# Kernel optimization log

Hardware: AMD Instinct MI355X
Metric: run time of the kernel (lower is better)

The kernel has to match this reference:

```python
import jax, jax.numpy as jnp
import numpy as np

LOOKBACK = 8
EPS = 1e-6
HID = 32
MV_DIM = 11  # 1 scalar + 4 vector + 6 bivector
# default bivector planes (i, j)
BIV_I = jnp.array([0, 0, 0, 1, 1, 2])
BIV_J = jnp.array([1, 2, 3, 2, 3, 3])


def phi(x):
    # LeakyReLU(x, 0.01) + 1.0
    return jnp.where(x >= 0, x, 0.01 * x) + 1.0


def setup_inputs() -> dict:
    key = jax.random.key(0)
    ks = jax.random.split(key, 10)
    B, L = 8, 16384
    return {
        "x": jax.random.normal(ks[0], (B, L, 4), dtype=jnp.float32),
        "scalar_bias": jax.random.normal(ks[1], (1,), dtype=jnp.float32) * 0.1,
        "vector_scale": 1.0 + jax.random.normal(ks[2], (4,), dtype=jnp.float32) * 0.1,
        "vector_bias": jax.random.normal(ks[3], (4,), dtype=jnp.float32) * 0.1,
        "bivector_weight": 1.0 + jax.random.normal(ks[4], (6,), dtype=jnp.float32) * 0.1,
        "W_Q": jax.random.normal(ks[5], (MV_DIM, HID), dtype=jnp.float32) * 0.3,
        "W_K": jax.random.normal(ks[6], (MV_DIM, HID), dtype=jnp.float32) * 0.3,
        "W_V": jax.random.normal(ks[7], (MV_DIM, HID), dtype=jnp.float32) * 0.3,
        "w_head": jax.random.normal(ks[8], (HID,), dtype=jnp.float32) * 0.18,
        "b_head": jax.random.normal(ks[9], (), dtype=jnp.float32) * 0.1,
    }


def ga_embed(x, scalar_bias, vector_scale, vector_bias, bivector_weight):
    B, L, _ = x.shape
    scalar = jnp.broadcast_to(1.0 + scalar_bias, (B, L, 1))  # [B,L,1]
    vec = x * vector_scale + vector_bias                      # [B,L,4]
    biv = bivector_weight * (x[..., BIV_I] - x[..., BIV_J])   # [B,L,6]
    return jnp.concatenate([scalar, vec, biv], axis=-1)       # [B,L,11]


def reference(x, scalar_bias, vector_scale, vector_bias, bivector_weight,
              W_Q, W_K, W_V, w_head, b_head):
    M = ga_embed(x, scalar_bias, vector_scale, vector_bias, bivector_weight)
    B, L, _ = M.shape
    Q = phi(M @ W_Q)  # [B,L,H]
    K = phi(M @ W_K)
    V = M @ W_V
    T = L - LOOKBACK
    # sliding windows: for output step t (t = LOOKBACK..L-1) window covers [t-Lb, t)
    win_idx = jnp.arange(T)[:, None] + jnp.arange(LOOKBACK)[None, :]  # [T,Lb]
    Kw = K[:, win_idx]  # [B,T,Lb,H]
    Vw = V[:, win_idx]  # [B,T,Lb,H]
    q = Q[:, LOOKBACK:, :]  # [B,T,H]
    # scores_l = q_t . k_l ; num = sum_l scores_l v_l ; den = sum_l scores_l
    # (identical math to q . (sum_l k_l v_l^T) and q . sum_l k_l)
    scores = jnp.einsum('bth,btlh->btl', q, Kw)               # [B,T,Lb]
    num = jnp.einsum('btl,btlg->btg', scores, Vw)             # [B,T,H]
    den = jnp.sum(scores, axis=-1, keepdims=True) + EPS
    contexts = num / den                                      # [B,T,H]
    weights = scores / (jnp.sum(scores, axis=-1, keepdims=True) + EPS)
    predictions = contexts @ w_head + b_head                  # [B,T]
    return predictions, weights
```

## Files before the change

### kernel.cpp

```cpp
#include <hip/hip_runtime.h>
#include <hip/hip_bf16.h>

#define LOOKBACK 8
#define HID 32
#define TB 256
#define NR  (TB + LOOKBACK)
#define RST 20
#define EPS 1e-6f

#define WS_AQ  0
#define WS_CQ  128
#define WS_AK  160
#define WS_CK  288
#define WS_AVW 320
#define WS_CVW 324
#define WS_N   336

__device__ __forceinline__ float phi1(float z) {
    return (z >= 0.0f ? z : 0.01f * z) + 1.0f;
}
__device__ __forceinline__ unsigned pack_bf16(float a, float b) {
    __hip_bfloat162 h = __float22bfloat162_rn(make_float2(a, b));
    return *reinterpret_cast<unsigned*>(&h);
}
__device__ __forceinline__ float blo(unsigned u) {
    return __uint_as_float(u << 16);
}
__device__ __forceinline__ float bhi(unsigned u) {
    return __uint_as_float(u & 0xffff0000u);
}

__global__ __launch_bounds__(TB) void ga_fused(
    const float* __restrict__ x,
    const float* __restrict__ sbp, const float* __restrict__ vsp,
    const float* __restrict__ vbp, const float* __restrict__ bwp,
    const float* __restrict__ WQ,  const float* __restrict__ WK,
    const float* __restrict__ WV,  const float* __restrict__ wh,
    const float* __restrict__ bhp,
    float* __restrict__ out,
    int B, int L)
{
    const int T   = L - LOOKBACK;
    const int bb  = blockIdx.y;
    const int t0  = blockIdx.x * TB;
    const int tid = threadIdx.x;

    __shared__ float    sP[WS_N];
    __shared__ unsigned sK[NR * RST];
    __shared__ float    sVW[NR];

    const float* xb = x + (size_t)bb * L * 4;

    const int t = t0 + tid;
    const bool valid = (t < T);
    const float4 xq = *reinterpret_cast<const float4*>(
        xb + (size_t)(valid ? t + LOOKBACK : 0) * 4);

    if (tid < 96) {
        const int h   = tid & 31;
        const int mat = tid >> 5;
        const float* W = (mat == 0) ? WQ : (mat == 1) ? WK : WV;
        float w[11];
#pragma unroll 1
        for (int j = 0; j < 11; ++j) w[j] = W[j * HID + h];

        const float b0 = bwp[0], b1 = bwp[1], b2 = bwp[2];
        const float b3 = bwp[3], b4 = bwp[4], b5 = bwp[5];
        const float v0 = vsp[0], v1 = vsp[1], v2 = vsp[2], v3 = vsp[3];
        const float u0 = vbp[0], u1 = vbp[1], u2 = vbp[2], u3 = vbp[3];
        const float s0 = 1.0f + sbp[0];

        const float a0 = v0*w[1] + b0*w[5] + b1*w[6] + b2*w[7];
        const float a1 = v1*w[2] - b0*w[5] + b3*w[8] + b4*w[9];
        const float a2 = v2*w[3] - b1*w[6] - b3*w[8] + b5*w[10];
        const float a3 = v3*w[4] - b2*w[7] - b4*w[9] - b5*w[10];
        const float c  = s0*w[0] + u0*w[1] + u1*w[2] + u2*w[3] + u3*w[4];

        if (mat == 0) {
            sP[WS_AQ + 0*HID + h] = a0; sP[WS_AQ + 1*HID + h] = a1;
            sP[WS_AQ + 2*HID + h] = a2; sP[WS_AQ + 3*HID + h] = a3;
            sP[WS_CQ + h] = c;
        } else if (mat == 1) {
            sP[WS_AK + 0*HID + h] = a0; sP[WS_AK + 1*HID + h] = a1;
            sP[WS_AK + 2*HID + h] = a2; sP[WS_AK + 3*HID + h] = a3;
            sP[WS_CK + h] = c;
        } else {
            const float ww = wh[h];
            float r[5] = { a0*ww, a1*ww, a2*ww, a3*ww, c*ww };
#pragma unroll
            for (int off = 16; off > 0; off >>= 1) {
#pragma unroll
                for (int i = 0; i < 5; ++i) r[i] += __shfl_down(r[i], off, 32);
            }
            if (h == 0) {
                sP[WS_AVW + 0] = r[0]; sP[WS_AVW + 1] = r[1];
                sP[WS_AVW + 2] = r[2]; sP[WS_AVW + 3] = r[3];
                sP[WS_CVW]     = r[4];
            }
        }
    }
    __syncthreads();

    const float avw0 = sP[WS_AVW + 0], avw1 = sP[WS_AVW + 1];
    const float avw2 = sP[WS_AVW + 2], avw3 = sP[WS_AVW + 3];
    const float cvw  = sP[WS_CVW];

    const int npos = min(NR, L - t0);
#pragma unroll 1
    for (int r = tid; r < npos; r += TB) {
        const float4 xv = *reinterpret_cast<const float4*>(xb + (size_t)(t0 + r) * 4);

        sVW[r] = cvw + xv.x*avw0 + xv.y*avw1 + xv.z*avw2 + xv.w*avw3;

        unsigned* dst = &sK[r * RST];
#pragma unroll 1
        for (int oc = 0; oc < 4; ++oc) {
            const int hb = oc * 8;
            const float4 c0 = *reinterpret_cast<const float4*>(&sP[WS_CK + hb]);
            const float4 c1 = *reinterpret_cast<const float4*>(&sP[WS_CK + hb + 4]);
            const float4 a0l = *reinterpret_cast<const float4*>(&sP[WS_AK + 0*HID + hb]);
            const float4 a0h = *reinterpret_cast<const float4*>(&sP[WS_AK + 0*HID + hb + 4]);
            const float4 a1l = *reinterpret_cast<const float4*>(&sP[WS_AK + 1*HID + hb]);
            const float4 a1h = *reinterpret_cast<const float4*>(&sP[WS_AK + 1*HID + hb + 4]);
            const float4 a2l = *reinterpret_cast<const float4*>(&sP[WS_AK + 2*HID + hb]);
            const float4 a2h = *reinterpret_cast<const float4*>(&sP[WS_AK + 2*HID + hb + 4]);
            const float4 a3l = *reinterpret_cast<const float4*>(&sP[WS_AK + 3*HID + hb]);
            const float4 a3h = *reinterpret_cast<const float4*>(&sP[WS_AK + 3*HID + hb + 4]);

            const float z0 = phi1(c0.x + xv.x*a0l.x + xv.y*a1l.x + xv.z*a2l.x + xv.w*a3l.x);
            const float z1 = phi1(c0.y + xv.x*a0l.y + xv.y*a1l.y + xv.z*a2l.y + xv.w*a3l.y);
            const float z2 = phi1(c0.z + xv.x*a0l.z + xv.y*a1l.z + xv.z*a2l.z + xv.w*a3l.z);
            const float z3 = phi1(c0.w + xv.x*a0l.w + xv.y*a1l.w + xv.z*a2l.w + xv.w*a3l.w);
            const float z4 = phi1(c1.x + xv.x*a0h.x + xv.y*a1h.x + xv.z*a2h.x + xv.w*a3h.x);
            const float z5 = phi1(c1.y + xv.x*a0h.y + xv.y*a1h.y + xv.z*a2h.y + xv.w*a3h.y);
            const float z6 = phi1(c1.z + xv.x*a0h.z + xv.y*a1h.z + xv.z*a2h.z + xv.w*a3h.z);
            const float z7 = phi1(c1.w + xv.x*a0h.w + xv.y*a1h.w + xv.z*a2h.w + xv.w*a3h.w);

            *reinterpret_cast<uint4*>(dst + oc*4) = make_uint4(
                pack_bf16(z0, z1), pack_bf16(z2, z3),
                pack_bf16(z4, z5), pack_bf16(z6, z7));
        }
    }
    __syncthreads();

    if (!valid) return;

    float sc[LOOKBACK];
#pragma unroll
    for (int l = 0; l < LOOKBACK; ++l) sc[l] = 0.0f;

#pragma unroll 1
    for (int oc = 0; oc < 4; ++oc) {
        const int hb = oc * 8;
        const float4 c0 = *reinterpret_cast<const float4*>(&sP[WS_CQ + hb]);
        const float4 c1 = *reinterpret_cast<const float4*>(&sP[WS_CQ + hb + 4]);
        const float4 a0l = *reinterpret_cast<const float4*>(&sP[WS_AQ + 0*HID + hb]);
        const float4 a0h = *reinterpret_cast<const float4*>(&sP[WS_AQ + 0*HID + hb + 4]);
        const float4 a1l = *reinterpret_cast<const float4*>(&sP[WS_AQ + 1*HID + hb]);
        const float4 a1h = *reinterpret_cast<const float4*>(&sP[WS_AQ + 1*HID + hb + 4]);
        const float4 a2l = *reinterpret_cast<const float4*>(&sP[WS_AQ + 2*HID + hb]);
        const float4 a2h = *reinterpret_cast<const float4*>(&sP[WS_AQ + 2*HID + hb + 4]);
        const float4 a3l = *reinterpret_cast<const float4*>(&sP[WS_AQ + 3*HID + hb]);
        const float4 a3h = *reinterpret_cast<const float4*>(&sP[WS_AQ + 3*HID + hb + 4]);

        const float q0 = phi1(c0.x + xq.x*a0l.x + xq.y*a1l.x + xq.z*a2l.x + xq.w*a3l.x);
        const float q1 = phi1(c0.y + xq.x*a0l.y + xq.y*a1l.y + xq.z*a2l.y + xq.w*a3l.y);
        const float q2 = phi1(c0.z + xq.x*a0l.z + xq.y*a1l.z + xq.z*a2l.z + xq.w*a3l.z);
        const float q3 = phi1(c0.w + xq.x*a0l.w + xq.y*a1l.w + xq.z*a2l.w + xq.w*a3l.w);
        const float q4 = phi1(c1.x + xq.x*a0h.x + xq.y*a1h.x + xq.z*a2h.x + xq.w*a3h.x);
        const float q5 = phi1(c1.y + xq.x*a0h.y + xq.y*a1h.y + xq.z*a2h.y + xq.w*a3h.y);
        const float q6 = phi1(c1.z + xq.x*a0h.z + xq.y*a1h.z + xq.z*a2h.z + xq.w*a3h.z);
        const float q7 = phi1(c1.w + xq.x*a0h.w + xq.y*a1h.w + xq.z*a2h.w + xq.w*a3h.w);

#pragma unroll
        for (int l = 0; l < LOOKBACK; ++l) {
            const uint4 w = *reinterpret_cast<const uint4*>(
                &sK[(tid + l) * RST + oc * 4]);
            sc[l] += blo(w.x)*q0 + bhi(w.x)*q1
                   + blo(w.y)*q2 + bhi(w.y)*q3
                   + blo(w.z)*q4 + bhi(w.z)*q5
                   + blo(w.w)*q6 + bhi(w.w)*q7;
        }
    }

    float ssum = 0.0f, p = 0.0f;
#pragma unroll
    for (int l = 0; l < LOOKBACK; ++l) {
        ssum += sc[l];
        p    += sc[l] * sVW[tid + l];
    }
    const float inv = 1.0f / (ssum + EPS);

    out[(size_t)bb * T + t] = p * inv + bhp[0];

    float* wout = out + (size_t)B * T + ((size_t)bb * T + t) * LOOKBACK;
    *reinterpret_cast<float4*>(wout) =
        make_float4(sc[0]*inv, sc[1]*inv, sc[2]*inv, sc[3]*inv);
    *reinterpret_cast<float4*>(wout + 4) =
        make_float4(sc[4]*inv, sc[5]*inv, sc[6]*inv, sc[7]*inv);
}

extern "C" void kernel_launch(void* const* d_in, const int* in_sizes, int n_in,
                              void* d_out, int out_size, void* d_ws, size_t ws_size,
                              hipStream_t stream) {
    const float* x  = (const float*)d_in[0];
    const float* sb = (const float*)d_in[1];
    const float* vs = (const float*)d_in[2];
    const float* vb = (const float*)d_in[3];
    const float* bw = (const float*)d_in[4];
    const float* WQ = (const float*)d_in[5];
    const float* WK = (const float*)d_in[6];
    const float* WV = (const float*)d_in[7];
    const float* wh = (const float*)d_in[8];
    const float* bh = (const float*)d_in[9];
    float* out = (float*)d_out;

    const long long bl = (long long)in_sizes[0] / 4;
    const long long bt = (long long)out_size / (1 + LOOKBACK);
    const int B = (int)((bl - bt) / LOOKBACK);
    const int L = (int)(bl / B);
    const int T = L - LOOKBACK;

    dim3 grid((T + TB - 1) / TB, B);
    ga_fused<<<grid, TB, 0, stream>>>(x, sb, vs, vb, bw, WQ, WK, WV, wh, bh,
                                      out, B, L);
}
```

Measured before the change: 15.50 us.

## Restructure kernel into single-wavefront blocks with 56 outputs per wave

Replaces the 256-thread blocks with 64-thread, single-wavefront blocks. Each lane computes one K row (with an overlap of 8 rows for the lookback), so each block produces 56 outputs. Weight-folding setup is spread across all 64 lanes, Q is kept as a 32-entry register array, and the scores loop reads full K rows. This is meant to cut the strided second pass and the large-block barrier costs, and to launch many more small blocks for better latency hiding. In exchange, the overlap rows are recomputed (64/56 extra K work), per-block setup is repeated far more often, and register pressure rises.

```diff
diff --git a/kernel.cpp b/kernel.cpp
--- a/kernel.cpp
+++ b/kernel.cpp
@@ -3,8 +3,7 @@
 
 #define LOOKBACK 8
 #define HID 32
-#define TB 256
-#define NR  (TB + LOOKBACK)
+#define TPW 56
 #define RST 20
 #define EPS 1e-6f
 
@@ -30,7 +29,7 @@
     return __uint_as_float(u & 0xffff0000u);
 }
 
-__global__ __launch_bounds__(TB) void ga_fused(
+__global__ __launch_bounds__(64) void ga_wave(
     const float* __restrict__ x,
     const float* __restrict__ sbp, const float* __restrict__ vsp,
     const float* __restrict__ vbp, const float* __restrict__ bwp,
@@ -40,29 +39,23 @@
     float* __restrict__ out,
     int B, int L)
 {
-    const int T   = L - LOOKBACK;
-    const int bb  = blockIdx.y;
-    const int t0  = blockIdx.x * TB;
-    const int tid = threadIdx.x;
+    const int T  = L - LOOKBACK;
+    const int bb = blockIdx.y;
+    const int t0 = blockIdx.x * TPW;
+    const int j  = threadIdx.x;
 
     __shared__ float    sP[WS_N];
-    __shared__ unsigned sK[NR * RST];
-    __shared__ float    sVW[NR];
+    __shared__ unsigned sK[64 * RST];
+    __shared__ float    sVW[64];
 
     const float* xb = x + (size_t)bb * L * 4;
 
-    const int t = t0 + tid;
-    const bool valid = (t < T);
-    const float4 xq = *reinterpret_cast<const float4*>(
-        xb + (size_t)(valid ? t + LOOKBACK : 0) * 4);
-
-    if (tid < 96) {
-        const int h   = tid & 31;
-        const int mat = tid >> 5;
-        const float* W = (mat == 0) ? WQ : (mat == 1) ? WK : WV;
+    const int ch = j & 31;
+    {
+        const float* W = (j < 32) ? WK : WQ;
         float w[11];
-#pragma unroll 1
-        for (int j = 0; j < 11; ++j) w[j] = W[j * HID + h];
+#pragma unroll
+        for (int i = 0; i < 11; ++i) w[i] = W[i * HID + ch];
 
         const float b0 = bwp[0], b1 = bwp[1], b2 = bwp[2];
         const float b3 = bwp[3], b4 = bwp[4], b5 = bwp[5];
@@ -76,80 +69,85 @@
         const float a3 = v3*w[4] - b2*w[7] - b4*w[9] - b5*w[10];
         const float c  = s0*w[0] + u0*w[1] + u1*w[2] + u2*w[3] + u3*w[4];
 
-        if (mat == 0) {
-            sP[WS_AQ + 0*HID + h] = a0; sP[WS_AQ + 1*HID + h] = a1;
-            sP[WS_AQ + 2*HID + h] = a2; sP[WS_AQ + 3*HID + h] = a3;
-            sP[WS_CQ + h] = c;
-        } else if (mat == 1) {
-            sP[WS_AK + 0*HID + h] = a0; sP[WS_AK + 1*HID + h] = a1;
-            sP[WS_AK + 2*HID + h] = a2; sP[WS_AK + 3*HID + h] = a3;
-            sP[WS_CK + h] = c;
-        } else {
-            const float ww = wh[h];
-            float r[5] = { a0*ww, a1*ww, a2*ww, a3*ww, c*ww };
-#pragma unroll
-            for (int off = 16; off > 0; off >>= 1) {
-#pragma unroll
-                for (int i = 0; i < 5; ++i) r[i] += __shfl_down(r[i], off, 32);
-            }
-            if (h == 0) {
-                sP[WS_AVW + 0] = r[0]; sP[WS_AVW + 1] = r[1];
-                sP[WS_AVW + 2] = r[2]; sP[WS_AVW + 3] = r[3];
-                sP[WS_CVW]     = r[4];
-            }
+        const int ab = (j < 32) ? WS_AK : WS_AQ;
+        const int cb = (j < 32) ? WS_CK : WS_CQ;
+        sP[ab + 0*HID + ch] = a0; sP[ab + 1*HID + ch] = a1;
+        sP[ab + 2*HID + ch] = a2; sP[ab + 3*HID + ch] = a3;
+        sP[cb + ch] = c;
+    }
+    if (j < 32) {
+        float w[11];
+#pragma unroll
+        for (int i = 0; i < 11; ++i) w[i] = WV[i * HID + ch];
+        const float b0 = bwp[0], b1 = bwp[1], b2 = bwp[2];
+        const float b3 = bwp[3], b4 = bwp[4], b5 = bwp[5];
+        const float v0 = vsp[0], v1 = vsp[1], v2 = vsp[2], v3 = vsp[3];
+        const float u0 = vbp[0], u1 = vbp[1], u2 = vbp[2], u3 = vbp[3];
+        const float s0 = 1.0f + sbp[0];
+
+        const float a0 = v0*w[1] + b0*w[5] + b1*w[6] + b2*w[7];
+        const float a1 = v1*w[2] - b0*w[5] + b3*w[8] + b4*w[9];
+        const float a2 = v2*w[3] - b1*w[6] - b3*w[8] + b5*w[10];
+        const float a3 = v3*w[4] - b2*w[7] - b4*w[9] - b5*w[10];
+        const float c  = s0*w[0] + u0*w[1] + u1*w[2] + u2*w[3] + u3*w[4];
+
+        const float ww = wh[ch];
+        float r0 = a0*ww, r1 = a1*ww, r2 = a2*ww, r3 = a3*ww, r4 = c*ww;
+#pragma unroll
+        for (int off = 16; off > 0; off >>= 1) {
+            r0 += __shfl_xor(r0, off, 64);
+            r1 += __shfl_xor(r1, off, 64);
+            r2 += __shfl_xor(r2, off, 64);
+            r3 += __shfl_xor(r3, off, 64);
+            r4 += __shfl_xor(r4, off, 64);
         }
+        if (ch == 0) {
+            sP[WS_AVW + 0] = r0; sP[WS_AVW + 1] = r1;
+            sP[WS_AVW + 2] = r2; sP[WS_AVW + 3] = r3;
+            sP[WS_CVW]     = r4;
+        }
     }
     __syncthreads();
 
-    const float avw0 = sP[WS_AVW + 0], avw1 = sP[WS_AVW + 1];
-    const float avw2 = sP[WS_AVW + 2], avw3 = sP[WS_AVW + 3];
-    const float cvw  = sP[WS_CVW];
-
-    const int npos = min(NR, L - t0);
-#pragma unroll 1
-    for (int r = tid; r < npos; r += TB) {
-        const float4 xv = *reinterpret_cast<const float4*>(xb + (size_t)(t0 + r) * 4);
-
-        sVW[r] = cvw + xv.x*avw0 + xv.y*avw1 + xv.z*avw2 + xv.w*avw3;
-
-        unsigned* dst = &sK[r * RST];
-#pragma unroll 1
-        for (int oc = 0; oc < 4; ++oc) {
-            const int hb = oc * 8;
-            const float4 c0 = *reinterpret_cast<const float4*>(&sP[WS_CK + hb]);
-            const float4 c1 = *reinterpret_cast<const float4*>(&sP[WS_CK + hb + 4]);
-            const float4 a0l = *reinterpret_cast<const float4*>(&sP[WS_AK + 0*HID + hb]);
-            const float4 a0h = *reinterpret_cast<const float4*>(&sP[WS_AK + 0*HID + hb + 4]);
-            const float4 a1l = *reinterpret_cast<const float4*>(&sP[WS_AK + 1*HID + hb]);
-            const float4 a1h = *reinterpret_cast<const float4*>(&sP[WS_AK + 1*HID + hb + 4]);
-            const float4 a2l = *reinterpret_cast<const float4*>(&sP[WS_AK + 2*HID + hb]);
-            const float4 a2h = *reinterpret_cast<const float4*>(&sP[WS_AK + 2*HID + hb + 4]);
-            const float4 a3l = *reinterpret_cast<const float4*>(&sP[WS_AK + 3*HID + hb]);
-            const float4 a3h = *reinterpret_cast<const float4*>(&sP[WS_AK + 3*HID + hb + 4]);
-
-            const float z0 = phi1(c0.x + xv.x*a0l.x + xv.y*a1l.x + xv.z*a2l.x + xv.w*a3l.x);
-            const float z1 = phi1(c0.y + xv.x*a0l.y + xv.y*a1l.y + xv.z*a2l.y + xv.w*a3l.y);
-            const float z2 = phi1(c0.z + xv.x*a0l.z + xv.y*a1l.z + xv.z*a2l.z + xv.w*a3l.z);
-            const float z3 = phi1(c0.w + xv.x*a0l.w + xv.y*a1l.w + xv.z*a2l.w + xv.w*a3l.w);
-            const float z4 = phi1(c1.x + xv.x*a0h.x + xv.y*a1h.x + xv.z*a2h.x + xv.w*a3h.x);
-            const float z5 = phi1(c1.y + xv.x*a0h.y + xv.y*a1h.y + xv.z*a2h.y + xv.w*a3h.y);
-            const float z6 = phi1(c1.z + xv.x*a0h.z + xv.y*a1h.z + xv.z*a2h.z + xv.w*a3h.z);
-            const float z7 = phi1(c1.w + xv.x*a0h.w + xv.y*a1h.w + xv.z*a2h.w + xv.w*a3h.w);
-
-            *reinterpret_cast<uint4*>(dst + oc*4) = make_uint4(
-                pack_bf16(z0, z1), pack_bf16(z2, z3),
-                pack_bf16(z4, z5), pack_bf16(z6, z7));
-        }
-    }
-    __syncthreads();
-
-    if (!valid) return;
-
-    float sc[LOOKBACK];
-#pragma unroll
-    for (int l = 0; l < LOOKBACK; ++l) sc[l] = 0.0f;
-
-#pragma unroll 1
+    const int rr = min(t0 + j, L - 1);
+    const float4 xv = *reinterpret_cast<const float4*>(xb + (size_t)rr * 4);
+    const int rq = min(t0 + j + LOOKBACK, L - 1);
+    const float4 xq = *reinterpret_cast<const float4*>(xb + (size_t)rq * 4);
+
+    sVW[j] = sP[WS_CVW] + xv.x*sP[WS_AVW+0] + xv.y*sP[WS_AVW+1]
+           + xv.z*sP[WS_AVW+2] + xv.w*sP[WS_AVW+3];
+
+    unsigned* dst = &sK[j * RST];
+#pragma unroll
+    for (int oc = 0; oc < 4; ++oc) {
+        const int hb = oc * 8;
+        const float4 c0 = *reinterpret_cast<const float4*>(&sP[WS_CK + hb]);
+        const float4 c1 = *reinterpret_cast<const float4*>(&sP[WS_CK + hb + 4]);
+        const float4 a0l = *reinterpret_cast<const float4*>(&sP[WS_AK + 0*HID + hb]);
+        const float4 a0h = *reinterpret_cast<const float4*>(&sP[WS_AK + 0*HID + hb + 4]);
+        const float4 a1l = *reinterpret_cast<const float4*>(&sP[WS_AK + 1*HID + hb]);
+        const float4 a1h = *reinterpret_cast<const float4*>(&sP[WS_AK + 1*HID + hb + 4]);
+        const float4 a2l = *reinterpret_cast<const float4*>(&sP[WS_AK + 2*HID + hb]);
+        const float4 a2h = *reinterpret_cast<const float4*>(&sP[WS_AK + 2*HID + hb + 4]);
+        const float4 a3l = *reinterpret_cast<const float4*>(&sP[WS_AK + 3*HID + hb]);
+        const float4 a3h = *reinterpret_cast<const float4*>(&sP[WS_AK + 3*HID + hb + 4]);
+
+        const float z0 = phi1(c0.x + xv.x*a0l.x + xv.y*a1l.x + xv.z*a2l.x + xv.w*a3l.x);
+        const float z1 = phi1(c0.y + xv.x*a0l.y + xv.y*a1l.y + xv.z*a2l.y + xv.w*a3l.y);
+        const float z2 = phi1(c0.z + xv.x*a0l.z + xv.y*a1l.z + xv.z*a2l.z + xv.w*a3l.z);
+        const float z3 = phi1(c0.w + xv.x*a0l.w + xv.y*a1l.w + xv.z*a2l.w + xv.w*a3l.w);
+        const float z4 = phi1(c1.x + xv.x*a0h.x + xv.y*a1h.x + xv.z*a2h.x + xv.w*a3h.x);
+        const float z5 = phi1(c1.y + xv.x*a0h.y + xv.y*a1h.y + xv.z*a2h.y + xv.w*a3h.y);
+        const float z6 = phi1(c1.z + xv.x*a0h.z + xv.y*a1h.z + xv.z*a2h.z + xv.w*a3h.z);
+        const float z7 = phi1(c1.w + xv.x*a0h.w + xv.y*a1h.w + xv.z*a2h.w + xv.w*a3h.w);
+
+        *reinterpret_cast<uint4*>(dst + oc*4) = make_uint4(
+            pack_bf16(z0, z1), pack_bf16(z2, z3),
+            pack_bf16(z4, z5), pack_bf16(z6, z7));
+    }
+
+    float q[HID];
+#pragma unroll
     for (int oc = 0; oc < 4; ++oc) {
         const int hb = oc * 8;
         const float4 c0 = *reinterpret_cast<const float4*>(&sP[WS_CQ + hb]);
@@ -163,41 +161,51 @@
         const float4 a3l = *reinterpret_cast<const float4*>(&sP[WS_AQ + 3*HID + hb]);
         const float4 a3h = *reinterpret_cast<const float4*>(&sP[WS_AQ + 3*HID + hb + 4]);
 
-        const float q0 = phi1(c0.x + xq.x*a0l.x + xq.y*a1l.x + xq.z*a2l.x + xq.w*a3l.x);
-        const float q1 = phi1(c0.y + xq.x*a0l.y + xq.y*a1l.y + xq.z*a2l.y + xq.w*a3l.y);
-        const float q2 = phi1(c0.z + xq.x*a0l.z + xq.y*a1l.z + xq.z*a2l.z + xq.w*a3l.z);
-        const float q3 = phi1(c0.w + xq.x*a0l.w + xq.y*a1l.w + xq.z*a2l.w + xq.w*a3l.w);
-        const float q4 = phi1(c1.x + xq.x*a0h.x + xq.y*a1h.x + xq.z*a2h.x + xq.w*a3h.x);
-        const float q5 = phi1(c1.y + xq.x*a0h.y + xq.y*a1h.y + xq.z*a2h.y + xq.w*a3h.y);
-        const float q6 = phi1(c1.z + xq.x*a0h.z + xq.y*a1h.z + xq.z*a2h.z + xq.w*a3h.z);
-        const float q7 = phi1(c1.w + xq.x*a0h.w + xq.y*a1h.w + xq.z*a2h.w + xq.w*a3h.w);
-
-#pragma unroll
-        for (int l = 0; l < LOOKBACK; ++l) {
-            const uint4 w = *reinterpret_cast<const uint4*>(
-                &sK[(tid + l) * RST + oc * 4]);
-            sc[l] += blo(w.x)*q0 + bhi(w.x)*q1
-                   + blo(w.y)*q2 + bhi(w.y)*q3
-                   + blo(w.z)*q4 + bhi(w.z)*q5
-                   + blo(w.w)*q6 + bhi(w.w)*q7;
-        }
-    }
-
+        q[hb+0] = phi1(c0.x + xq.x*a0l.x + xq.y*a1l.x + xq.z*a2l.x + xq.w*a3l.x);
+        q[hb+1] = phi1(c0.y + xq.x*a0l.y + xq.y*a1l.y + xq.z*a2l.y + xq.w*a3l.y);
+        q[hb+2] = phi1(c0.z + xq.x*a0l.z + xq.y*a1l.z + xq.z*a2l.z + xq.w*a3l.z);
+        q[hb+3] = phi1(c0.w + xq.x*a0l.w + xq.y*a1l.w + xq.z*a2l.w + xq.w*a3l.w);
+        q[hb+4] = phi1(c1.x + xq.x*a0h.x + xq.y*a1h.x + xq.z*a2h.x + xq.w*a3h.x);
+        q[hb+5] = phi1(c1.y + xq.x*a0h.y + xq.y*a1h.y + xq.z*a2h.y + xq.w*a3h.y);
+        q[hb+6] = phi1(c1.z + xq.x*a0h.z + xq.y*a1h.z + xq.z*a2h.z + xq.w*a3h.z);
+        q[hb+7] = phi1(c1.w + xq.x*a0h.w + xq.y*a1h.w + xq.z*a2h.w + xq.w*a3h.w);
+    }
+    __syncthreads();
+
+    float sc[LOOKBACK];
     float ssum = 0.0f, p = 0.0f;
 #pragma unroll
     for (int l = 0; l < LOOKBACK; ++l) {
-        ssum += sc[l];
-        p    += sc[l] * sVW[tid + l];
+        const int ri = min(j + l, 63);
+        const unsigned* kr = &sK[ri * RST];
+        const uint4 w0 = *reinterpret_cast<const uint4*>(kr);
+        const uint4 w1 = *reinterpret_cast<const uint4*>(kr + 4);
+        const uint4 w2 = *reinterpret_cast<const uint4*>(kr + 8);
+        const uint4 w3 = *reinterpret_cast<const uint4*>(kr + 12);
+        float s;
+        s  = blo(w0.x)*q[0]  + bhi(w0.x)*q[1]  + blo(w0.y)*q[2]  + bhi(w0.y)*q[3];
+        s += blo(w0.z)*q[4]  + bhi(w0.z)*q[5]  + blo(w0.w)*q[6]  + bhi(w0.w)*q[7];
+        s += blo(w1.x)*q[8]  + bhi(w1.x)*q[9]  + blo(w1.y)*q[10] + bhi(w1.y)*q[11];
+        s += blo(w1.z)*q[12] + bhi(w1.z)*q[13] + blo(w1.w)*q[14] + bhi(w1.w)*q[15];
+        s += blo(w2.x)*q[16] + bhi(w2.x)*q[17] + blo(w2.y)*q[18] + bhi(w2.y)*q[19];
+        s += blo(w2.z)*q[20] + bhi(w2.z)*q[21] + blo(w2.w)*q[22] + bhi(w2.w)*q[23];
+        s += blo(w3.x)*q[24] + bhi(w3.x)*q[25] + blo(w3.y)*q[26] + bhi(w3.y)*q[27];
+        s += blo(w3.z)*q[28] + bhi(w3.z)*q[29] + blo(w3.w)*q[30] + bhi(w3.w)*q[31];
+        sc[l] = s;
+        ssum += s;
+        p += s * sVW[ri];
     }
     const float inv = 1.0f / (ssum + EPS);
 
-    out[(size_t)bb * T + t] = p * inv + bhp[0];
-
-    float* wout = out + (size_t)B * T + ((size_t)bb * T + t) * LOOKBACK;
-    *reinterpret_cast<float4*>(wout) =
-        make_float4(sc[0]*inv, sc[1]*inv, sc[2]*inv, sc[3]*inv);
-    *reinterpret_cast<float4*>(wout + 4) =
-        make_float4(sc[4]*inv, sc[5]*inv, sc[6]*inv, sc[7]*inv);
+    const int t = t0 + j;
+    if (j < TPW && t < T) {
+        out[(size_t)bb * T + t] = p * inv + bhp[0];
+        float* wout = out + (size_t)B * T + ((size_t)bb * T + t) * LOOKBACK;
+        *reinterpret_cast<float4*>(wout) =
+            make_float4(sc[0]*inv, sc[1]*inv, sc[2]*inv, sc[3]*inv);
+        *reinterpret_cast<float4*>(wout + 4) =
+            make_float4(sc[4]*inv, sc[5]*inv, sc[6]*inv, sc[7]*inv);
+    }
 }
 
 extern "C" void kernel_launch(void* const* d_in, const int* in_sizes, int n_in,
@@ -221,7 +229,7 @@
     const int L = (int)(bl / B);
     const int T = L - LOOKBACK;
 
-    dim3 grid((T + TB - 1) / TB, B);
-    ga_fused<<<grid, TB, 0, stream>>>(x, sb, vs, vb, bw, WQ, WK, WV, wh, bh,
-                                      out, B, L);
-}
+    dim3 grid((T + TPW - 1) / TPW, B);
+    ga_wave<<<grid, 64, 0, stream>>>(x, sb, vs, vb, bw, WQ, WK, WV, wh, bh,
+                                     out, B, L);
+}
```

New measurement: 15.99 us. +3.2%, slower.
